# Performance work log

Measured on AMD Instinct MI355X. Metric: run time of the kernel, lower is better.

Reference implementation:

```python
import jax, jax.numpy as jnp
import numpy as np

B, G, D, S, NEG = 64, 7, 1280, 5, 16  # batch, grid=7, pred_size=1280, pred_steps, neg_samples
SAME = NEG // 5                        # same-image negatives, as in torch code
CELLS = G * G                          # 49 cells per image


def _step_counts():
    return [B * (G - 1 - s) * G for s in range(S)]  # rows in [0, 6-s), 7 cols


def _make_indices(rng):
    """Precompute the random negative-sample indices the torch loop draws on the fly.
    Returns ctx_idx [P] (flat index into contexts) and cand_idx [P, NEG+1]
    (flat indices into encodings; column 0 is the positive target)."""
    ctx_list, cand_list = [], []
    for s in range(S):
        rows, cols, imgs = np.arange(G - 1 - s), np.arange(G), np.arange(B)
        im, ro, co = np.meshgrid(imgs, rows, cols, indexing='ij')
        im, ro, co = im.ravel(), ro.ravel(), co.ravel()          # [Ps]
        ctx_list.append(im * CELLS + ro * G + co)
        tgt_cell = (ro + s + 1) * G + co                          # pred_row = row+step+1
        tgt = im * CELLS + tgt_cell
        # same-image negatives: any cell except the target cell
        r = rng.integers(0, CELLS - 1, size=(im.size, SAME))
        cell = r + (r >= tgt_cell[:, None])
        neg_same = im[:, None] * CELLS + cell
        # cross-image negatives: any other image, any cell
        ri = rng.integers(0, B - 1, size=(im.size, NEG - SAME))
        img_n = ri + (ri >= im[:, None])
        neg_cross = img_n * CELLS + rng.integers(0, CELLS, size=(im.size, NEG - SAME))
        cand_list.append(np.concatenate([tgt[:, None], neg_same, neg_cross], axis=1))
    return (np.concatenate(ctx_list).astype(np.int32),
            np.concatenate(cand_list, axis=0).astype(np.int32))


def setup_inputs() -> dict:
    key = jax.random.key(0)
    k1, k2, k3, k4 = jax.random.split(key, 4)
    rng = np.random.default_rng(0)
    ctx_idx, cand_idx = _make_indices(rng)
    return {
        'contexts': jax.random.normal(k1, (B, G, G, D), jnp.float32),
        'encodings': jax.random.normal(k2, (B, G, G, D), jnp.float32),
        'Wk_w': jax.random.normal(k3, (S, D, D), jnp.float32) * (1.0 / np.sqrt(D)),
        'Wk_b': jax.random.normal(k4, (S, D), jnp.float32) * 0.01,
        'ctx_idx': jnp.asarray(ctx_idx),
        'cand_idx': jnp.asarray(cand_idx),
    }


def reference(contexts, encodings, Wk_w, Wk_b, ctx_idx, cand_idx):
    ctx_flat = contexts.reshape(-1, D)   # [B*49, D]
    enc_flat = encodings.reshape(-1, D)  # [B*49, D]
    offs = np.concatenate([[0], np.cumsum(_step_counts())])
    P = int(offs[-1])
    total_loss = jnp.float32(0.0)
    total_correct = jnp.float32(0.0)
    for s in range(S):  # fixed small loop over pred_steps
        ci = ctx_idx[offs[s]:offs[s + 1]]                 # [Ps]
        ki = cand_idx[offs[s]:offs[s + 1]]                # [Ps, NEG+1]
        c = ctx_flat[ci]                                  # [Ps, D]
        pred = c @ Wk_w[s].T + Wk_b[s]                    # nn.Linear: x W^T + b
        cand = enc_flat[ki]                               # [Ps, NEG+1, D]
        dots = jnp.einsum('pd,pkd->pk', pred, cand)       # [Ps, NEG+1]
        total_loss = total_loss + (-jax.nn.log_softmax(dots, axis=-1)[:, 0]).sum()
        total_correct = total_correct + (jnp.argmax(dots, axis=-1) == 0).astype(jnp.float32).sum()
    return total_loss / P, total_correct / P
```

## Files before the change

### kernel.cpp

```cpp
#include <hip/hip_runtime.h>

#define DD 1280
#define PP 8960
#define NK 17
#define NCTX 4014080
#define NW   8192000
#define NBLK 2240

typedef __attribute__((ext_vector_type(8))) short bf16x8;
typedef __attribute__((ext_vector_type(4))) float f32x4;
typedef __attribute__((ext_vector_type(2))) float f32x2;
typedef unsigned short u16;
typedef unsigned char u8;

__device__ __forceinline__ u16 f2bf(float f) {
  union { float f; unsigned u; } v; v.f = f;
  unsigned r = v.u + 0x7fffu + ((v.u >> 16) & 1u);
  return (u16)(r >> 16);
}
__device__ __forceinline__ float bf2f(u16 h) {
  union { unsigned u; float f; } v; v.u = ((unsigned)h) << 16;
  return v.f;
}

__device__ __forceinline__ void gload16(const u16* g, const u16* l) {
  __builtin_amdgcn_global_load_lds(
      (const __attribute__((address_space(1))) unsigned*)g,
      (__attribute__((address_space(3))) unsigned*)l, 16, 0, 0);
}

__global__ __launch_bounds__(256) void k_cvt3(const float* __restrict__ ctx,
                                              const float* __restrict__ enc,
                                              const float* __restrict__ Ww,
                                              u16* __restrict__ ctx_bf,
                                              u8*  __restrict__ enc_f8,
                                              u16* __restrict__ W_bf) {
  const int b = blockIdx.x;
  if (b >= 3920 && b < 7840) {
    const int i = ((b - 3920) * 256 + threadIdx.x) * 4;
    float4 v = *reinterpret_cast<const float4*>(enc + i);
    unsigned u = __builtin_amdgcn_cvt_pk_fp8_f32(v.x, v.y, 0u, false);
    u = __builtin_amdgcn_cvt_pk_fp8_f32(v.z, v.w, u, true);
    *reinterpret_cast<unsigned*>(enc_f8 + i) = u;
    return;
  }
  const float* src; u16* dst; int i;
  if (b < 3920) { src = ctx; dst = ctx_bf; i = (b * 256 + threadIdx.x) * 4; }
  else          { src = Ww;  dst = W_bf;   i = ((b - 7840) * 256 + threadIdx.x) * 4; }
  float4 v = *reinterpret_cast<const float4*>(src + i);
  ushort4 o;
  o.x = f2bf(v.x); o.y = f2bf(v.y); o.z = f2bf(v.z); o.w = f2bf(v.w);
  *reinterpret_cast<ushort4*>(dst + i) = o;
}

__global__ __launch_bounds__(256) void k_gemm(const u16* __restrict__ ctx,
                                              const u16* __restrict__ W,
                                              const float* __restrict__ Wb,
                                              const int* __restrict__ cidx,
                                              u16* __restrict__ pred) {
  __shared__ u16 SM[17408];

  const int id  = blockIdx.x;
  const int xcd = id & 7, pos = id >> 3;
  const int wgid = (xcd < 6) ? (xcd * 89 + pos) : (534 + (xcd - 6) * 88 + pos);
  const int bx = wgid / 10;
  const int by = wgid - bx * 10;

  int s, mt0, off, mend;
  if (bx < 21)      { s = 0; mt0 = 0;  off = 0;    mend = 2688; }
  else if (bx < 39) { s = 1; mt0 = 21; off = 2688; mend = 4928; }
  else if (bx < 53) { s = 2; mt0 = 39; off = 4928; mend = 6720; }
  else if (bx < 64) { s = 3; mt0 = 53; off = 6720; mend = 8064; }
  else              { s = 4; mt0 = 64; off = 8064; mend = 8960; }
  const int m0 = off + (bx - mt0) * 128;
  const int n0 = by * 128;

  const int t = threadIdx.x;
  const int lane = t & 63, wid = t >> 6;
  const int wr = wid >> 1, wc = wid & 1;
  const int lr = lane & 15, kq = lane >> 4;

  const int r0s = t >> 2, c0 = t & 3;
  const int r1s = 64 + r0s;
  const int cs0 = c0 ^ ((r0s >> 1) & 3);
  const int cs1 = c0 ^ ((r1s >> 1) & 3);
  int ar0 = m0 + r0s; if (ar0 > mend - 1) ar0 = mend - 1;
  int ar1 = m0 + r1s; if (ar1 > mend - 1) ar1 = mend - 1;
  const u16* aptr0 = ctx + (size_t)cidx[ar0] * DD + cs0 * 8;
  const u16* aptr1 = ctx + (size_t)cidx[ar1] * DD + cs1 * 8;
  const u16* bbase = W + (size_t)s * DD * DD;
  const u16* bptr0 = bbase + (size_t)(n0 + r0s) * DD + cs0 * 8;
  const u16* bptr1 = bbase + (size_t)(n0 + r1s) * DD + cs1 * 8;
  const int sl0 = wid * 512;
  const int sl1 = 2048 + wid * 512;

  f32x4 acc[4][4];
  #pragma unroll
  for (int i = 0; i < 4; ++i)
    #pragma unroll
    for (int j = 0; j < 4; ++j)
      acc[i][j] = (f32x4){0.f, 0.f, 0.f, 0.f};

  int aoff[4], boff[4];
  #pragma unroll
  for (int mi = 0; mi < 4; ++mi) {
    const int ra = wr * 64 + mi * 16 + lr;
    aoff[mi] = ra * 32 + (kq ^ ((ra >> 1) & 3)) * 8;
  }
  #pragma unroll
  for (int ni = 0; ni < 4; ++ni) {
    const int rb = wc * 64 + ni * 16 + lr;
    boff[ni] = rb * 32 + (kq ^ ((rb >> 1) & 3)) * 8;
  }

  gload16(aptr0, SM + sl0); gload16(aptr1, SM + sl1);
  gload16(bptr0, SM + 8192 + sl0); gload16(bptr1, SM + 8192 + sl1);

  #pragma unroll 2
  for (int kt = 0; kt < 40; ++kt) {
    const int cur = kt & 1;
    if (kt < 39) {
      const int k0 = (kt + 1) * 32;
      const int d = (cur ^ 1) * 4096;
      gload16(aptr0 + k0, SM + d + sl0); gload16(aptr1 + k0, SM + d + sl1);
      gload16(bptr0 + k0, SM + 8192 + d + sl0); gload16(bptr1 + k0, SM + 8192 + d + sl1);
      asm volatile("s_waitcnt vmcnt(4)" ::: "memory");
    } else {
      asm volatile("s_waitcnt vmcnt(0)" ::: "memory");
    }
    __builtin_amdgcn_s_barrier();
    __builtin_amdgcn_sched_barrier(0);

    const u16* ab = SM + cur * 4096;
    const u16* bb = SM + 8192 + cur * 4096;
    bf16x8 af[4], bf[4];
    #pragma unroll
    for (int mi = 0; mi < 4; ++mi)
      af[mi] = *reinterpret_cast<const bf16x8*>(ab + aoff[mi]);
    #pragma unroll
    for (int ni = 0; ni < 4; ++ni)
      bf[ni] = *reinterpret_cast<const bf16x8*>(bb + boff[ni]);
    #pragma unroll
    for (int mi = 0; mi < 4; ++mi)
      #pragma unroll
      for (int ni = 0; ni < 4; ++ni)
        acc[mi][ni] = __builtin_amdgcn_mfma_f32_16x16x32_bf16(af[mi], bf[ni], acc[mi][ni], 0, 0, 0);

    __builtin_amdgcn_sched_barrier(0);
    __builtin_amdgcn_s_barrier();
  }

  if (m0 + wr * 64 < mend) {
    u16* cs = SM + wid * 4352;
    const float* bias = Wb + s * DD;
    #pragma unroll
    for (int ni = 0; ni < 4; ++ni) {
      const float bv = bias[n0 + wc * 64 + ni * 16 + lr];
      #pragma unroll
      for (int mi = 0; mi < 4; ++mi) {
        #pragma unroll
        for (int i = 0; i < 4; ++i)
          cs[(mi * 16 + kq * 4 + i) * 68 + ni * 16 + lr] = f2bf(acc[mi][ni][i] + bv);
      }
    }
    asm volatile("s_waitcnt lgkmcnt(0)" ::: "memory");
    __builtin_amdgcn_sched_barrier(0);
    const int rl = lane >> 3, ch = lane & 7;
    #pragma unroll
    for (int it = 0; it < 8; ++it) {
      const int row = it * 8 + rl;
      bf16x8 v = *reinterpret_cast<const bf16x8*>(cs + row * 68 + ch * 8);
      *reinterpret_cast<bf16x8*>(pred + (size_t)(m0 + wr * 64 + row) * DD
                                 + n0 + wc * 64 + ch * 8) = v;
    }
  }
}

__global__ __launch_bounds__(256) void k_dots(const u16* __restrict__ pred,
                                              const u8* __restrict__ enc8,
                                              const int* __restrict__ kidx,
                                              float* __restrict__ ploss,
                                              float* __restrict__ pcorr) {
  const int wid  = threadIdx.x >> 6;
  const int lane = threadIdx.x & 63;
  const int p    = blockIdx.x * 4 + wid;

  const u16* prow = pred + (size_t)p * DD + lane * 4;
  float pr[20];
  #pragma unroll
  for (int j = 0; j < 5; ++j) {
    ushort4 v = *reinterpret_cast<const ushort4*>(prow + j * 256);
    pr[j * 4 + 0] = bf2f(v.x);
    pr[j * 4 + 1] = bf2f(v.y);
    pr[j * 4 + 2] = bf2f(v.z);
    pr[j * 4 + 3] = bf2f(v.w);
  }

  float dots[NK];
  #pragma unroll
  for (int kb = 0; kb < NK; kb += 5) {
    const int nb = (NK - kb < 5) ? (NK - kb) : 5;
    unsigned eu[5][5];
    #pragma unroll
    for (int kk = 0; kk < 5; ++kk)
      if (kk < nb) {
        const u8* erow = enc8 + (size_t)kidx[p * NK + kb + kk] * DD + lane * 4;
        #pragma unroll
        for (int j = 0; j < 5; ++j)
          eu[kk][j] = *reinterpret_cast<const unsigned*>(erow + j * 256);
      }
    #pragma unroll
    for (int kk = 0; kk < 5; ++kk)
      if (kk < nb) {
        float sum = 0.f;
        #pragma unroll
        for (int j = 0; j < 5; ++j) {
          f32x2 lo = __builtin_amdgcn_cvt_pk_f32_fp8(eu[kk][j], false);
          f32x2 hi = __builtin_amdgcn_cvt_pk_f32_fp8(eu[kk][j], true);
          sum += pr[j * 4 + 0] * lo[0] + pr[j * 4 + 1] * lo[1]
               + pr[j * 4 + 2] * hi[0] + pr[j * 4 + 3] * hi[1];
        }
        #pragma unroll
        for (int off = 32; off >= 1; off >>= 1) sum += __shfl_xor(sum, off, 64);
        dots[kb + kk] = sum;
      }
  }

  float mx = dots[0];
  #pragma unroll
  for (int k = 1; k < NK; ++k) mx = fmaxf(mx, dots[k]);
  float se = 0.f;
  #pragma unroll
  for (int k = 0; k < NK; ++k) se += __expf(dots[k] - mx);
  const float loss = __logf(se) + mx - dots[0];
  const float corr = (dots[0] == mx) ? 1.f : 0.f;

  __shared__ float sl[4], sc[4];
  if (lane == 0) { sl[wid] = loss; sc[wid] = corr; }
  __syncthreads();
  if (threadIdx.x == 0) {
    ploss[blockIdx.x] = sl[0] + sl[1] + sl[2] + sl[3];
    pcorr[blockIdx.x] = sc[0] + sc[1] + sc[2] + sc[3];
  }
}

__global__ __launch_bounds__(256) void k_red(const float* __restrict__ ploss,
                                             const float* __restrict__ pcorr,
                                             float* __restrict__ out) {
  float l = 0.f, c = 0.f;
  for (int i = threadIdx.x; i < NBLK; i += 256) { l += ploss[i]; c += pcorr[i]; }
  #pragma unroll
  for (int off = 32; off >= 1; off >>= 1) {
    l += __shfl_xor(l, off, 64);
    c += __shfl_xor(c, off, 64);
  }
  __shared__ float sl[4], sc[4];
  const int wid = threadIdx.x >> 6, lane = threadIdx.x & 63;
  if (lane == 0) { sl[wid] = l; sc[wid] = c; }
  __syncthreads();
  if (threadIdx.x == 0) {
    out[0] = (sl[0] + sl[1] + sl[2] + sl[3]) * (1.0f / PP);
    out[1] = (sc[0] + sc[1] + sc[2] + sc[3]) * (1.0f / PP);
  }
}

extern "C" void kernel_launch(void* const* d_in, const int* in_sizes, int n_in,
                              void* d_out, int out_size, void* d_ws, size_t ws_size,
                              hipStream_t stream) {
  (void)in_sizes; (void)n_in; (void)out_size; (void)ws_size;

  const float* ctx_f = (const float*)d_in[0];
  const float* enc_f = (const float*)d_in[1];
  const float* Ww    = (const float*)d_in[2];
  const float* Wb    = (const float*)d_in[3];
  const int*   cidx  = (const int*)d_in[4];
  const int*   kidx  = (const int*)d_in[5];
  float* out = (float*)d_out;

  char* ws = (char*)d_ws;
  u16* ctx_bf = (u16*)(ws);
  u8*  enc_f8 = (u8*)(ws + 8028160);
  u16* W_bf   = (u16*)(ws + 16056320);
  u16* pred   = (u16*)(ws + 32440320);
  float* ploss = (float*)(ws + 55377920);
  float* pcorr = (float*)(ws + 55377920 + 8960);

  k_cvt3<<<dim3(15840), 256, 0, stream>>>(ctx_f, enc_f, Ww, ctx_bf, enc_f8, W_bf);

  k_gemm<<<dim3(710), 256, 0, stream>>>(ctx_bf, W_bf, Wb, cidx, pred);

  k_dots<<<dim3(NBLK), 256, 0, stream>>>(pred, enc_f8, kidx, ploss, pcorr);

  k_red<<<dim3(1), 256, 0, stream>>>(ploss, pcorr, out);
}
```

Before: 166.5 us.

## Triple-buffer GEMM K-loop LDS staging to prefetch two tiles ahead

Changes the GEMM main loop from double-buffered to triple-buffered LDS, issuing global-to-LDS loads two K-steps ahead and waiting with vmcnt(8) instead of vmcnt(4). This keeps more loads in flight to hide global memory latency behind the MFMA work. In exchange, LDS use per block grows from about 34 KB to 48 KB, which may lower occupancy, and the two tail iterations are peeled out of the loop. The rotating slot indices add a little scalar bookkeeping.

```diff
diff --git a/kernel.cpp b/kernel.cpp
--- a/kernel.cpp
+++ b/kernel.cpp
@@ -58,7 +58,7 @@
                                               const float* __restrict__ Wb,
                                               const int* __restrict__ cidx,
                                               u16* __restrict__ pred) {
-  __shared__ u16 SM[17408];
+  __shared__ u16 SM[24576];
 
   const int id  = blockIdx.x;
   const int xcd = id & 7, pos = id >> 3;
@@ -113,26 +113,9 @@
     boff[ni] = rb * 32 + (kq ^ ((rb >> 1) & 3)) * 8;
   }
 
-  gload16(aptr0, SM + sl0); gload16(aptr1, SM + sl1);
-  gload16(bptr0, SM + 8192 + sl0); gload16(bptr1, SM + 8192 + sl1);
-
-  #pragma unroll 2
-  for (int kt = 0; kt < 40; ++kt) {
-    const int cur = kt & 1;
-    if (kt < 39) {
-      const int k0 = (kt + 1) * 32;
-      const int d = (cur ^ 1) * 4096;
-      gload16(aptr0 + k0, SM + d + sl0); gload16(aptr1 + k0, SM + d + sl1);
-      gload16(bptr0 + k0, SM + 8192 + d + sl0); gload16(bptr1 + k0, SM + 8192 + d + sl1);
-      asm volatile("s_waitcnt vmcnt(4)" ::: "memory");
-    } else {
-      asm volatile("s_waitcnt vmcnt(0)" ::: "memory");
-    }
-    __builtin_amdgcn_s_barrier();
-    __builtin_amdgcn_sched_barrier(0);
-
-    const u16* ab = SM + cur * 4096;
-    const u16* bb = SM + 8192 + cur * 4096;
+  auto compute = [&](int slot) {
+    const u16* ab = SM + slot * 4096;
+    const u16* bb = SM + 12288 + slot * 4096;
     bf16x8 af[4], bf[4];
     #pragma unroll
     for (int mi = 0; mi < 4; ++mi)
@@ -145,10 +128,41 @@
       #pragma unroll
       for (int ni = 0; ni < 4; ++ni)
         acc[mi][ni] = __builtin_amdgcn_mfma_f32_16x16x32_bf16(af[mi], bf[ni], acc[mi][ni], 0, 0, 0);
-
+  };
+
+  gload16(aptr0, SM + sl0);               gload16(aptr1, SM + sl1);
+  gload16(bptr0, SM + 12288 + sl0);       gload16(bptr1, SM + 12288 + sl1);
+  gload16(aptr0 + 32, SM + 4096 + sl0);   gload16(aptr1 + 32, SM + 4096 + sl1);
+  gload16(bptr0 + 32, SM + 16384 + sl0);  gload16(bptr1 + 32, SM + 16384 + sl1);
+
+  int rd = 0, st = 2;
+  #pragma unroll 2
+  for (int kt = 0; kt < 38; ++kt) {
+    const int k0 = (kt + 2) * 32;
+    const int da = st * 4096, db = 12288 + st * 4096;
+    gload16(aptr0 + k0, SM + da + sl0); gload16(aptr1 + k0, SM + da + sl1);
+    gload16(bptr0 + k0, SM + db + sl0); gload16(bptr1 + k0, SM + db + sl1);
+    asm volatile("s_waitcnt vmcnt(8)" ::: "memory");
+    __builtin_amdgcn_s_barrier();
+    __builtin_amdgcn_sched_barrier(0);
+    compute(rd);
     __builtin_amdgcn_sched_barrier(0);
     __builtin_amdgcn_s_barrier();
-  }
+    rd = (rd == 2) ? 0 : rd + 1;
+    st = (st == 2) ? 0 : st + 1;
+  }
+  asm volatile("s_waitcnt vmcnt(4)" ::: "memory");
+  __builtin_amdgcn_s_barrier();
+  __builtin_amdgcn_sched_barrier(0);
+  compute(2);
+  __builtin_amdgcn_sched_barrier(0);
+  __builtin_amdgcn_s_barrier();
+  asm volatile("s_waitcnt vmcnt(0)" ::: "memory");
+  __builtin_amdgcn_s_barrier();
+  __builtin_amdgcn_sched_barrier(0);
+  compute(0);
+  __builtin_amdgcn_sched_barrier(0);
+  __builtin_amdgcn_s_barrier();
 
   if (m0 + wr * 64 < mend) {
     u16* cs = SM + wid * 4352;
```

After: 172.5 us. 3.6% more time.

## Overlap encoding FP8 conversion with GEMM and fold final reduction into dots

Applied to the files above, without the earlier changes.

The encodings-to-FP8 conversion moves out of the conversion kernel and into extra blocks appended to the GEMM launch, so it runs alongside the GEMM tiles instead of ahead of them. The separate single-block reduction kernel is removed. The last dots block, detected with an atomic counter that the conversion kernel resets, now sums the partials. This saves one launch and shortens the conversion stage, at the cost of extra blocks competing with GEMM tiles for CUs and an atomic per dots block.

```diff
diff --git a/kernel.cpp b/kernel.cpp
--- a/kernel.cpp
+++ b/kernel.cpp
@@ -29,36 +29,39 @@
       (__attribute__((address_space(3))) unsigned*)l, 16, 0, 0);
 }
 
-__global__ __launch_bounds__(256) void k_cvt3(const float* __restrict__ ctx,
+__global__ __launch_bounds__(256) void k_cvt(const float* __restrict__ ctx,
+                                             const float* __restrict__ Ww,
+                                             u16* __restrict__ ctx_bf,
+                                             u16* __restrict__ W_bf,
+                                             unsigned* __restrict__ cnt) {
+  const int b = blockIdx.x;
+  if (b == 0 && threadIdx.x == 0) *cnt = 0u;
+  const float* src; u16* dst; int i;
+  if (b < 3920) { src = ctx; dst = ctx_bf; i = (b * 256 + threadIdx.x) * 4; }
+  else          { src = Ww;  dst = W_bf;   i = ((b - 3920) * 256 + threadIdx.x) * 4; }
+  float4 v = *reinterpret_cast<const float4*>(src + i);
+  ushort4 o;
+  o.x = f2bf(v.x); o.y = f2bf(v.y); o.z = f2bf(v.z); o.w = f2bf(v.w);
+  *reinterpret_cast<ushort4*>(dst + i) = o;
+}
+
+__global__ __launch_bounds__(256) void k_gemm(const u16* __restrict__ ctx,
+                                              const u16* __restrict__ W,
+                                              const float* __restrict__ Wb,
+                                              const int* __restrict__ cidx,
+                                              u16* __restrict__ pred,
                                               const float* __restrict__ enc,
-                                              const float* __restrict__ Ww,
-                                              u16* __restrict__ ctx_bf,
-                                              u8*  __restrict__ enc_f8,
-                                              u16* __restrict__ W_bf) {
-  const int b = blockIdx.x;
-  if (b >= 3920 && b < 7840) {
-    const int i = ((b - 3920) * 256 + threadIdx.x) * 4;
+                                              u8* __restrict__ enc_f8) {
+  __shared__ u16 SM[17408];
+
+  if (blockIdx.x >= 710) {
+    const int i = ((blockIdx.x - 710) * 256 + threadIdx.x) * 4;
     float4 v = *reinterpret_cast<const float4*>(enc + i);
     unsigned u = __builtin_amdgcn_cvt_pk_fp8_f32(v.x, v.y, 0u, false);
     u = __builtin_amdgcn_cvt_pk_fp8_f32(v.z, v.w, u, true);
     *reinterpret_cast<unsigned*>(enc_f8 + i) = u;
     return;
   }
-  const float* src; u16* dst; int i;
-  if (b < 3920) { src = ctx; dst = ctx_bf; i = (b * 256 + threadIdx.x) * 4; }
-  else          { src = Ww;  dst = W_bf;   i = ((b - 7840) * 256 + threadIdx.x) * 4; }
-  float4 v = *reinterpret_cast<const float4*>(src + i);
-  ushort4 o;
-  o.x = f2bf(v.x); o.y = f2bf(v.y); o.z = f2bf(v.z); o.w = f2bf(v.w);
-  *reinterpret_cast<ushort4*>(dst + i) = o;
-}
-
-__global__ __launch_bounds__(256) void k_gemm(const u16* __restrict__ ctx,
-                                              const u16* __restrict__ W,
-                                              const float* __restrict__ Wb,
-                                              const int* __restrict__ cidx,
-                                              u16* __restrict__ pred) {
-  __shared__ u16 SM[17408];
 
   const int id  = blockIdx.x;
   const int xcd = id & 7, pos = id >> 3;
@@ -180,7 +183,9 @@
                                               const u8* __restrict__ enc8,
                                               const int* __restrict__ kidx,
                                               float* __restrict__ ploss,
-                                              float* __restrict__ pcorr) {
+                                              float* __restrict__ pcorr,
+                                              unsigned* __restrict__ cnt,
+                                              float* __restrict__ out) {
   const int wid  = threadIdx.x >> 6;
   const int lane = threadIdx.x & 63;
   const int p    = blockIdx.x * 4 + wid;
@@ -236,26 +241,31 @@
   const float corr = (dots[0] == mx) ? 1.f : 0.f;
 
   __shared__ float sl[4], sc[4];
+  __shared__ int last;
   if (lane == 0) { sl[wid] = loss; sc[wid] = corr; }
   __syncthreads();
   if (threadIdx.x == 0) {
-    ploss[blockIdx.x] = sl[0] + sl[1] + sl[2] + sl[3];
-    pcorr[blockIdx.x] = sc[0] + sc[1] + sc[2] + sc[3];
-  }
-}
-
-__global__ __launch_bounds__(256) void k_red(const float* __restrict__ ploss,
-                                             const float* __restrict__ pcorr,
-                                             float* __restrict__ out) {
+    const float L = sl[0] + sl[1] + sl[2] + sl[3];
+    const float C = sc[0] + sc[1] + sc[2] + sc[3];
+    __hip_atomic_store(&ploss[blockIdx.x], L, __ATOMIC_RELAXED, __HIP_MEMORY_SCOPE_AGENT);
+    __hip_atomic_store(&pcorr[blockIdx.x], C, __ATOMIC_RELAXED, __HIP_MEMORY_SCOPE_AGENT);
+    const unsigned prev =
+        __hip_atomic_fetch_add(cnt, 1u, __ATOMIC_ACQ_REL, __HIP_MEMORY_SCOPE_AGENT);
+    last = (prev == NBLK - 1);
+  }
+  __syncthreads();
+  if (!last) return;
+
   float l = 0.f, c = 0.f;
-  for (int i = threadIdx.x; i < NBLK; i += 256) { l += ploss[i]; c += pcorr[i]; }
+  for (int i = threadIdx.x; i < NBLK; i += 256) {
+    l += __hip_atomic_load(&ploss[i], __ATOMIC_RELAXED, __HIP_MEMORY_SCOPE_AGENT);
+    c += __hip_atomic_load(&pcorr[i], __ATOMIC_RELAXED, __HIP_MEMORY_SCOPE_AGENT);
+  }
   #pragma unroll
   for (int off = 32; off >= 1; off >>= 1) {
     l += __shfl_xor(l, off, 64);
     c += __shfl_xor(c, off, 64);
   }
-  __shared__ float sl[4], sc[4];
-  const int wid = threadIdx.x >> 6, lane = threadIdx.x & 63;
   if (lane == 0) { sl[wid] = l; sc[wid] = c; }
   __syncthreads();
   if (threadIdx.x == 0) {
@@ -284,12 +294,11 @@
   u16* pred   = (u16*)(ws + 32440320);
   float* ploss = (float*)(ws + 55377920);
   float* pcorr = (float*)(ws + 55377920 + 8960);
-
-  k_cvt3<<<dim3(15840), 256, 0, stream>>>(ctx_f, enc_f, Ww, ctx_bf, enc_f8, W_bf);
-
-  k_gemm<<<dim3(710), 256, 0, stream>>>(ctx_bf, W_bf, Wb, cidx, pred);
-
-  k_dots<<<dim3(NBLK), 256, 0, stream>>>(pred, enc_f8, kidx, ploss, pcorr);
-
-  k_red<<<dim3(1), 256, 0, stream>>>(ploss, pcorr, out);
-}
+  unsigned* cnt = (unsigned*)(ws + 55377920 + 17920);
+
+  k_cvt<<<dim3(11920), 256, 0, stream>>>(ctx_f, Ww, ctx_bf, W_bf, cnt);
+
+  k_gemm<<<dim3(4630), 256, 0, stream>>>(ctx_bf, W_bf, Wb, cidx, pred, enc_f, enc_f8);
+
+  k_dots<<<dim3(NBLK), 256, 0, stream>>>(pred, enc_f8, kidx, ploss, pcorr, cnt, out);
+}
```

After: 196.8 us. 18.2% more time.

## Split each prediction's 17 candidate dots across four waves in k_dots

Applied to the files above, without the earlier changes.

k_dots previously gave one wave per prediction, walking all 17 candidate rows in serial batches of five. Now each block handles one prediction, and its four waves take 5/4/4/4 candidates each, so all candidate loads are issued at once. The dots go through shared memory and wave 0 does a lane-parallel softmax/argmax. This raises memory-level parallelism and the block count, at the cost of loading each pred row four times, a block barrier, and a longer final reduction over 8960 partials.

```diff
diff --git a/kernel.cpp b/kernel.cpp
--- a/kernel.cpp
+++ b/kernel.cpp
@@ -5,7 +5,6 @@
 #define NK 17
 #define NCTX 4014080
 #define NW   8192000
-#define NBLK 2240
 
 typedef __attribute__((ext_vector_type(8))) short bf16x8;
 typedef __attribute__((ext_vector_type(4))) float f32x4;
@@ -181,9 +180,18 @@
                                               const int* __restrict__ kidx,
                                               float* __restrict__ ploss,
                                               float* __restrict__ pcorr) {
+  __shared__ float sdots[20];
   const int wid  = threadIdx.x >> 6;
   const int lane = threadIdx.x & 63;
-  const int p    = blockIdx.x * 4 + wid;
+  const int p    = blockIdx.x;
+
+  const int cst = (wid == 0) ? 0 : (1 + wid * 4);
+  const int cnt = (wid == 0) ? 5 : 4;
+
+  int ki[5];
+  #pragma unroll
+  for (int kk = 0; kk < 5; ++kk)
+    if (kk < cnt) ki[kk] = kidx[p * NK + cst + kk];
 
   const u16* prow = pred + (size_t)p * DD + lane * 4;
   float pr[20];
@@ -196,51 +204,45 @@
     pr[j * 4 + 3] = bf2f(v.w);
   }
 
-  float dots[NK];
-  #pragma unroll
-  for (int kb = 0; kb < NK; kb += 5) {
-    const int nb = (NK - kb < 5) ? (NK - kb) : 5;
-    unsigned eu[5][5];
-    #pragma unroll
-    for (int kk = 0; kk < 5; ++kk)
-      if (kk < nb) {
-        const u8* erow = enc8 + (size_t)kidx[p * NK + kb + kk] * DD + lane * 4;
-        #pragma unroll
-        for (int j = 0; j < 5; ++j)
-          eu[kk][j] = *reinterpret_cast<const unsigned*>(erow + j * 256);
+  unsigned eu[5][5];
+  #pragma unroll
+  for (int kk = 0; kk < 5; ++kk)
+    if (kk < cnt) {
+      const u8* erow = enc8 + (size_t)ki[kk] * DD + lane * 4;
+      #pragma unroll
+      for (int j = 0; j < 5; ++j)
+        eu[kk][j] = *reinterpret_cast<const unsigned*>(erow + j * 256);
+    }
+  #pragma unroll
+  for (int kk = 0; kk < 5; ++kk)
+    if (kk < cnt) {
+      float sum = 0.f;
+      #pragma unroll
+      for (int j = 0; j < 5; ++j) {
+        f32x2 lo = __builtin_amdgcn_cvt_pk_f32_fp8(eu[kk][j], false);
+        f32x2 hi = __builtin_amdgcn_cvt_pk_f32_fp8(eu[kk][j], true);
+        sum += pr[j * 4 + 0] * lo[0] + pr[j * 4 + 1] * lo[1]
+             + pr[j * 4 + 2] * hi[0] + pr[j * 4 + 3] * hi[1];
       }
-    #pragma unroll
-    for (int kk = 0; kk < 5; ++kk)
-      if (kk < nb) {
-        float sum = 0.f;
-        #pragma unroll
-        for (int j = 0; j < 5; ++j) {
-          f32x2 lo = __builtin_amdgcn_cvt_pk_f32_fp8(eu[kk][j], false);
-          f32x2 hi = __builtin_amdgcn_cvt_pk_f32_fp8(eu[kk][j], true);
-          sum += pr[j * 4 + 0] * lo[0] + pr[j * 4 + 1] * lo[1]
-               + pr[j * 4 + 2] * hi[0] + pr[j * 4 + 3] * hi[1];
-        }
-        #pragma unroll
-        for (int off = 32; off >= 1; off >>= 1) sum += __shfl_xor(sum, off, 64);
-        dots[kb + kk] = sum;
-      }
-  }
-
-  float mx = dots[0];
-  #pragma unroll
-  for (int k = 1; k < NK; ++k) mx = fmaxf(mx, dots[k]);
-  float se = 0.f;
-  #pragma unroll
-  for (int k = 0; k < NK; ++k) se += __expf(dots[k] - mx);
-  const float loss = __logf(se) + mx - dots[0];
-  const float corr = (dots[0] == mx) ? 1.f : 0.f;
-
-  __shared__ float sl[4], sc[4];
-  if (lane == 0) { sl[wid] = loss; sc[wid] = corr; }
+      #pragma unroll
+      for (int off = 32; off >= 1; off >>= 1) sum += __shfl_xor(sum, off, 64);
+      if (lane == 0) sdots[cst + kk] = sum;
+    }
+
   __syncthreads();
-  if (threadIdx.x == 0) {
-    ploss[blockIdx.x] = sl[0] + sl[1] + sl[2] + sl[3];
-    pcorr[blockIdx.x] = sc[0] + sc[1] + sc[2] + sc[3];
+  if (wid != 0) return;
+
+  const float d0 = sdots[0];
+  float v = (lane < NK) ? sdots[lane] : -1e30f;
+  float mx = v;
+  #pragma unroll
+  for (int off = 32; off >= 1; off >>= 1) mx = fmaxf(mx, __shfl_xor(mx, off, 64));
+  float e = (lane < NK) ? __expf(v - mx) : 0.f;
+  #pragma unroll
+  for (int off = 32; off >= 1; off >>= 1) e += __shfl_xor(e, off, 64);
+  if (lane == 0) {
+    ploss[p] = __logf(e) + mx - d0;
+    pcorr[p] = (d0 == mx) ? 1.f : 0.f;
   }
 }
 
@@ -248,7 +250,7 @@
                                              const float* __restrict__ pcorr,
                                              float* __restrict__ out) {
   float l = 0.f, c = 0.f;
-  for (int i = threadIdx.x; i < NBLK; i += 256) { l += ploss[i]; c += pcorr[i]; }
+  for (int i = threadIdx.x; i < PP; i += 256) { l += ploss[i]; c += pcorr[i]; }
   #pragma unroll
   for (int off = 32; off >= 1; off >>= 1) {
     l += __shfl_xor(l, off, 64);
@@ -283,13 +285,13 @@
   u16* W_bf   = (u16*)(ws + 16056320);
   u16* pred   = (u16*)(ws + 32440320);
   float* ploss = (float*)(ws + 55377920);
-  float* pcorr = (float*)(ws + 55377920 + 8960);
+  float* pcorr = (float*)(ws + 55377920 + 35840);
 
   k_cvt3<<<dim3(15840), 256, 0, stream>>>(ctx_f, enc_f, Ww, ctx_bf, enc_f8, W_bf);
 
   k_gemm<<<dim3(710), 256, 0, stream>>>(ctx_bf, W_bf, Wb, cidx, pred);
 
-  k_dots<<<dim3(NBLK), 256, 0, stream>>>(pred, enc_f8, kidx, ploss, pcorr);
+  k_dots<<<dim3(PP), 256, 0, stream>>>(pred, enc_f8, kidx, ploss, pcorr);
 
   k_red<<<dim3(1), 256, 0, stream>>>(ploss, pcorr, out);
 }
```

New measurement: 172.9 us. 1.04x slower.
